# Performance work log

Measured on AMD Instinct MI355X. Metric: run time of the kernel, lower is better.

Reference implementation:

```python
import jax, jax.numpy as jnp
import numpy as np

W_NBITS = 8
A_NBITS = 8


def _fake_quant_weight_per_channel(w, nbits):
    # symmetric per-output-channel (row) fake quantization
    qmax = float(2 ** (nbits - 1) - 1)
    scale = jnp.max(jnp.abs(w), axis=1, keepdims=True) / qmax  # [out, 1]
    scale = jnp.maximum(scale, 1e-8)
    return jnp.clip(jnp.round(w / scale), -qmax - 1.0, qmax) * scale


def _fake_quant_act_per_group(x, group_size, nbits):
    # dynamic symmetric per-group fake quantization along the feature dim
    qmax = float(2 ** (nbits - 1) - 1)
    tokens, feat = x.shape
    xg = x.reshape(tokens, feat // group_size, group_size)
    scale = jnp.max(jnp.abs(xg), axis=-1, keepdims=True) / qmax  # [T, G, 1]
    scale = jnp.maximum(scale, 1e-8)
    xq = jnp.clip(jnp.round(xg / scale), -qmax - 1.0, qmax) * scale
    return xq.reshape(tokens, feat)


def setup_inputs() -> dict:
    key = jax.random.key(0)
    k1, k2, k3 = jax.random.split(key, 3)
    tokens, in_f, out_f = 8192, 4096, 4096
    x = jax.random.normal(k1, (tokens, in_f), dtype=jnp.float32)
    weight = jax.random.normal(k2, (out_f, in_f), dtype=jnp.float32) * 0.02
    bias = jax.random.normal(k3, (out_f,), dtype=jnp.float32) * 0.02
    return {"x": x, "weight": weight, "bias": bias, "group_size": 128}


def reference(x, weight, bias, group_size):
    w_q = _fake_quant_weight_per_channel(weight, W_NBITS)
    x_q = _fake_quant_act_per_group(x, group_size, A_NBITS)
    # F.linear: x @ w.T + b
    return jnp.einsum("tc,oc->to", x_q, w_q) + bias
```

## Files before the change

### kernel.cpp

```cpp
#include <hip/hip_runtime.h>
#include <stdint.h>


typedef __attribute__((ext_vector_type(4))) int   i32x4;
typedef __attribute__((ext_vector_type(4))) float f32x4;

static __device__ __forceinline__ void load_lds16(const void* g, void* l) {
    __builtin_amdgcn_global_load_lds(
        (const __attribute__((address_space(1))) void*)g,
        (__attribute__((address_space(3))) void*)l, 16, 0, 0);
}

static __device__ __forceinline__ int8_t q8(float v, float scale) {
    float q = rintf(v / scale);
    q = fminf(fmaxf(q, -128.0f), 127.0f);
    return (int8_t)(int)q;
}

__global__ __launch_bounds__(256) void quant_fused_kernel(
        const float* __restrict__ x, int8_t* __restrict__ xq,
        float* __restrict__ sxT,
        const float* __restrict__ w, int8_t* __restrict__ wq,
        float* __restrict__ sw, int in_f, int M) {
    const int b = blockIdx.x, t = threadIdx.x;
    if (b < M) {
        const int row = b;
        const float* xr = x + (size_t)row * in_f;
        int8_t* xo = xq + (size_t)row * in_f;
        for (int base = t * 4; base < in_f; base += 256 * 4) {
            float4 v = *(const float4*)(xr + base);
            float m = fmaxf(fmaxf(fabsf(v.x), fabsf(v.y)),
                            fmaxf(fabsf(v.z), fabsf(v.w)));
            m = fmaxf(m, __shfl_xor(m, 1));
            m = fmaxf(m, __shfl_xor(m, 2));
            m = fmaxf(m, __shfl_xor(m, 4));
            m = fmaxf(m, __shfl_xor(m, 8));
            m = fmaxf(m, __shfl_xor(m, 16));
            const float scale = fmaxf(m / 127.0f, 1e-8f);
            char4 o;
            o.x = q8(v.x, scale); o.y = q8(v.y, scale);
            o.z = q8(v.z, scale); o.w = q8(v.w, scale);
            *(char4*)(xo + base) = o;
            if ((t & 31) == 0)
                sxT[(size_t)(base >> 7) * M + row] = scale;
        }
    } else {
        const int row = b - M;
        const float* wr = w + (size_t)row * in_f;
        int8_t* wo = wq + (size_t)row * in_f;
        float4 v[4];
        float m = 0.0f;
#pragma unroll
        for (int i = 0; i < 4; i++) {
            v[i] = *(const float4*)(wr + t * 4 + i * 1024);
            m = fmaxf(m, fmaxf(fmaxf(fabsf(v[i].x), fabsf(v[i].y)),
                               fmaxf(fabsf(v[i].z), fabsf(v[i].w))));
        }
#pragma unroll
        for (int off = 1; off < 64; off <<= 1)
            m = fmaxf(m, __shfl_xor(m, off));
        __shared__ float wm[4];
        if ((t & 63) == 0) wm[t >> 6] = m;
        __syncthreads();
        m = fmaxf(fmaxf(wm[0], wm[1]), fmaxf(wm[2], wm[3]));
        const float scale = fmaxf(m / 127.0f, 1e-8f);
        if (t == 0) sw[row] = scale;
#pragma unroll
        for (int i = 0; i < 4; i++) {
            char4 o;
            o.x = q8(v[i].x, scale); o.y = q8(v[i].y, scale);
            o.z = q8(v[i].z, scale); o.w = q8(v[i].w, scale);
            *(char4*)(wo + t * 4 + i * 1024) = o;
        }
    }
}

__global__ __launch_bounds__(256, 2) void gemm_i8_kernel(
        const int8_t* __restrict__ A, const int8_t* __restrict__ B,
        const float* __restrict__ sxT, const float* __restrict__ sw,
        const float* __restrict__ bias, float* __restrict__ C,
        int M, int N, int K) {
    __shared__ __align__(16) int8_t As[128 * 128];
    __shared__ __align__(16) int8_t Bs[128 * 128];
    const int tid = threadIdx.x;
    const int wave = tid >> 6, lane = tid & 63;
    const int bm = blockIdx.y * 128, bn = blockIdx.x * 128;
    const int wm = (wave >> 1) * 64, wn = (wave & 1) * 64;

    f32x4 acc[4][4];
#pragma unroll
    for (int i = 0; i < 4; i++)
#pragma unroll
        for (int j = 0; j < 4; j++) acc[i][j] = (f32x4){0.f, 0.f, 0.f, 0.f};

    const int srow = wave * 8 + (lane >> 3);
    const int scol = (((lane & 7) ^ ((lane >> 3) & 7)) * 16);
    const size_t sK = (size_t)K;
    const int8_t* Ag = A + (size_t)(bm + srow) * sK + scol;
    const int8_t* Bg = B + (size_t)(bn + srow) * sK + scol;
    int8_t* AsW = As + (wave * 8) * 128;
    int8_t* BsW = Bs + (wave * 8) * 128;

    const int fr = lane & 15, q = lane >> 4, r7 = lane & 7;
    const float* sxg = sxT + bm + wm + q * 4;

    for (int k0 = 0; k0 < K; k0 += 128) {
#pragma unroll
        for (int i = 0; i < 4; i++) {
            load_lds16(Ag + k0 + (size_t)i * 32 * sK, AsW + i * 32 * 128);
            load_lds16(Bg + k0 + (size_t)i * 32 * sK, BsW + i * 32 * 128);
        }
        f32x4 sxv[4];
#pragma unroll
        for (int mi = 0; mi < 4; mi++)
            sxv[mi] = *(const f32x4*)(sxg + (size_t)(k0 >> 7) * M + mi * 16);
        __syncthreads();

        i32x4 a[4][2], b[4][2];
#pragma unroll
        for (int mi = 0; mi < 4; mi++) {
            const int arow = wm + mi * 16 + fr;
            const int brow = wn + mi * 16 + fr;
#pragma unroll
            for (int h = 0; h < 2; h++) {
                a[mi][h] = *(const i32x4*)(As + arow * 128 +
                                           ((h * 4 + q) ^ r7) * 16);
                b[mi][h] = *(const i32x4*)(Bs + brow * 128 +
                                           ((h * 4 + q) ^ r7) * 16);
            }
        }
#pragma unroll
        for (int mi = 0; mi < 4; mi++)
#pragma unroll
            for (int ni = 0; ni < 4; ni++) {
                i32x4 iacc = __builtin_amdgcn_mfma_i32_16x16x64_i8(
                    a[mi][0], b[ni][0], (i32x4){0, 0, 0, 0}, 0, 0, 0);
                iacc = __builtin_amdgcn_mfma_i32_16x16x64_i8(
                    a[mi][1], b[ni][1], iacc, 0, 0, 0);
#pragma unroll
                for (int r = 0; r < 4; r++)
                    acc[mi][ni][r] += (float)iacc[r] * sxv[mi][r];
            }
        __syncthreads();
    }

    const int or0 = bm + wm + q * 4;
    const int oc0 = bn + wn + fr;
    float swv[4], bv[4];
#pragma unroll
    for (int ni = 0; ni < 4; ni++) {
        swv[ni] = sw[oc0 + ni * 16];
        bv[ni] = bias[oc0 + ni * 16];
    }
#pragma unroll
    for (int mi = 0; mi < 4; mi++)
#pragma unroll
        for (int ni = 0; ni < 4; ni++)
#pragma unroll
            for (int r = 0; r < 4; r++)
                C[(size_t)(or0 + mi * 16 + r) * N + (oc0 + ni * 16)] =
                    acc[mi][ni][r] * swv[ni] + bv[ni];
}

extern "C" void kernel_launch(void* const* d_in, const int* in_sizes, int n_in,
                              void* d_out, int out_size, void* d_ws, size_t ws_size,
                              hipStream_t stream) {
    const float* x    = (const float*)d_in[0];
    const float* w    = (const float*)d_in[1];
    const float* bias = (const float*)d_in[2];

    const int out_f  = in_sizes[2];
    const int in_f   = in_sizes[1] / out_f;
    const int tokens = in_sizes[0] / in_f;
    const int G = in_f / 128;

    int8_t* xq  = (int8_t*)d_ws;
    int8_t* wq  = xq + (size_t)tokens * in_f;
    float*  sxT = (float*)(wq + (size_t)out_f * in_f);
    float*  sw  = sxT + (size_t)G * tokens;
    float*  out = (float*)d_out;

    quant_fused_kernel<<<tokens + out_f, 256, 0, stream>>>(
        x, xq, sxT, w, wq, sw, in_f, tokens);

    dim3 grid(out_f / 128, tokens / 128);
    gemm_i8_kernel<<<grid, 256, 0, stream>>>(xq, wq, sxT, sw, bias, out,
                                             tokens, out_f, in_f);
}
```

Measured before the change: 446.0 us.

## Split quant kernel and vectorize per-thread 16-element loads with reciprocal scale

Splits the fused quantization into separate activation and weight kernels. Each thread now loads 16 contiguous floats and writes one 16-byte int8 vector. The group reduction for activations shrinks to 3 shuffles, and the per-element divide is replaced by multiplying with a reciprocal. Sizes are hardcoded to 4096 features, and the reciprocal multiply may round a few values differently from the divide in the reference.

```diff
diff --git a/kernel.cpp b/kernel.cpp
--- a/kernel.cpp
+++ b/kernel.cpp
@@ -11,68 +11,77 @@
         (__attribute__((address_space(3))) void*)l, 16, 0, 0);
 }
 
-static __device__ __forceinline__ int8_t q8(float v, float scale) {
-    float q = rintf(v / scale);
+static __device__ __forceinline__ int8_t q8m(float v, float inv) {
+    float q = rintf(v * inv);
     q = fminf(fmaxf(q, -128.0f), 127.0f);
     return (int8_t)(int)q;
 }
 
-__global__ __launch_bounds__(256) void quant_fused_kernel(
+__global__ __launch_bounds__(256) void quant_act_kernel(
         const float* __restrict__ x, int8_t* __restrict__ xq,
-        float* __restrict__ sxT,
+        float* __restrict__ sxT, int M) {
+    const int row = blockIdx.x, t = threadIdx.x;
+    const float* xr = x + (size_t)row * 4096;
+    float4 v[4];
+#pragma unroll
+    for (int i = 0; i < 4; i++)
+        v[i] = *(const float4*)(xr + t * 16 + i * 4);
+    float m = 0.0f;
+#pragma unroll
+    for (int i = 0; i < 4; i++)
+        m = fmaxf(m, fmaxf(fmaxf(fabsf(v[i].x), fabsf(v[i].y)),
+                           fmaxf(fabsf(v[i].z), fabsf(v[i].w))));
+    m = fmaxf(m, __shfl_xor(m, 1));
+    m = fmaxf(m, __shfl_xor(m, 2));
+    m = fmaxf(m, __shfl_xor(m, 4));
+    const float scale = fmaxf(m / 127.0f, 1e-8f);
+    const float inv = 1.0f / scale;
+    union { int8_t b[16]; i32x4 w; } o;
+#pragma unroll
+    for (int i = 0; i < 4; i++) {
+        o.b[i * 4 + 0] = q8m(v[i].x, inv);
+        o.b[i * 4 + 1] = q8m(v[i].y, inv);
+        o.b[i * 4 + 2] = q8m(v[i].z, inv);
+        o.b[i * 4 + 3] = q8m(v[i].w, inv);
+    }
+    *(i32x4*)(xq + (size_t)row * 4096 + t * 16) = o.w;
+    if ((t & 7) == 0)
+        sxT[(size_t)(t >> 3) * M + row] = scale;
+}
+
+__global__ __launch_bounds__(256) void quant_wgt_kernel(
         const float* __restrict__ w, int8_t* __restrict__ wq,
-        float* __restrict__ sw, int in_f, int M) {
-    const int b = blockIdx.x, t = threadIdx.x;
-    if (b < M) {
-        const int row = b;
-        const float* xr = x + (size_t)row * in_f;
-        int8_t* xo = xq + (size_t)row * in_f;
-        for (int base = t * 4; base < in_f; base += 256 * 4) {
-            float4 v = *(const float4*)(xr + base);
-            float m = fmaxf(fmaxf(fabsf(v.x), fabsf(v.y)),
-                            fmaxf(fabsf(v.z), fabsf(v.w)));
-            m = fmaxf(m, __shfl_xor(m, 1));
-            m = fmaxf(m, __shfl_xor(m, 2));
-            m = fmaxf(m, __shfl_xor(m, 4));
-            m = fmaxf(m, __shfl_xor(m, 8));
-            m = fmaxf(m, __shfl_xor(m, 16));
-            const float scale = fmaxf(m / 127.0f, 1e-8f);
-            char4 o;
-            o.x = q8(v.x, scale); o.y = q8(v.y, scale);
-            o.z = q8(v.z, scale); o.w = q8(v.w, scale);
-            *(char4*)(xo + base) = o;
-            if ((t & 31) == 0)
-                sxT[(size_t)(base >> 7) * M + row] = scale;
-        }
-    } else {
-        const int row = b - M;
-        const float* wr = w + (size_t)row * in_f;
-        int8_t* wo = wq + (size_t)row * in_f;
-        float4 v[4];
-        float m = 0.0f;
+        float* __restrict__ sw) {
+    const int row = blockIdx.x, t = threadIdx.x;
+    const float* wr = w + (size_t)row * 4096;
+    float4 v[4];
 #pragma unroll
-        for (int i = 0; i < 4; i++) {
-            v[i] = *(const float4*)(wr + t * 4 + i * 1024);
-            m = fmaxf(m, fmaxf(fmaxf(fabsf(v[i].x), fabsf(v[i].y)),
-                               fmaxf(fabsf(v[i].z), fabsf(v[i].w))));
-        }
+    for (int i = 0; i < 4; i++)
+        v[i] = *(const float4*)(wr + t * 16 + i * 4);
+    float m = 0.0f;
 #pragma unroll
-        for (int off = 1; off < 64; off <<= 1)
-            m = fmaxf(m, __shfl_xor(m, off));
-        __shared__ float wm[4];
-        if ((t & 63) == 0) wm[t >> 6] = m;
-        __syncthreads();
-        m = fmaxf(fmaxf(wm[0], wm[1]), fmaxf(wm[2], wm[3]));
-        const float scale = fmaxf(m / 127.0f, 1e-8f);
-        if (t == 0) sw[row] = scale;
+    for (int i = 0; i < 4; i++)
+        m = fmaxf(m, fmaxf(fmaxf(fabsf(v[i].x), fabsf(v[i].y)),
+                           fmaxf(fabsf(v[i].z), fabsf(v[i].w))));
 #pragma unroll
-        for (int i = 0; i < 4; i++) {
-            char4 o;
-            o.x = q8(v[i].x, scale); o.y = q8(v[i].y, scale);
-            o.z = q8(v[i].z, scale); o.w = q8(v[i].w, scale);
-            *(char4*)(wo + t * 4 + i * 1024) = o;
-        }
+    for (int off = 1; off < 64; off <<= 1)
+        m = fmaxf(m, __shfl_xor(m, off));
+    __shared__ float wm[4];
+    if ((t & 63) == 0) wm[t >> 6] = m;
+    __syncthreads();
+    m = fmaxf(fmaxf(wm[0], wm[1]), fmaxf(wm[2], wm[3]));
+    const float scale = fmaxf(m / 127.0f, 1e-8f);
+    if (t == 0) sw[row] = scale;
+    const float inv = 1.0f / scale;
+    union { int8_t b[16]; i32x4 w4; } o;
+#pragma unroll
+    for (int i = 0; i < 4; i++) {
+        o.b[i * 4 + 0] = q8m(v[i].x, inv);
+        o.b[i * 4 + 1] = q8m(v[i].y, inv);
+        o.b[i * 4 + 2] = q8m(v[i].z, inv);
+        o.b[i * 4 + 3] = q8m(v[i].w, inv);
     }
+    *(i32x4*)(wq + (size_t)row * 4096 + t * 16) = o.w4;
 }
 
 __global__ __launch_bounds__(256, 2) void gemm_i8_kernel(
@@ -180,8 +189,8 @@
     float*  sw  = sxT + (size_t)G * tokens;
     float*  out = (float*)d_out;
 
-    quant_fused_kernel<<<tokens + out_f, 256, 0, stream>>>(
-        x, xq, sxT, w, wq, sw, in_f, tokens);
+    quant_act_kernel<<<tokens, 256, 0, stream>>>(x, xq, sxT, tokens);
+    quant_wgt_kernel<<<out_f, 256, 0, stream>>>(w, wq, sw);
 
     dim3 grid(out_f / 128, tokens / 128);
     gemm_i8_kernel<<<grid, 256, 0, stream>>>(xq, wq, sxT, sw, bias, out,
```

New measurement: 445.8 us. Within noise of the previous version (-0.0%).
